# Kernel tuning notes

Measured on AMD Instinct MI355X. Metric: run time of the kernel, lower is better.

## Reference

```python
import jax, jax.numpy as jnp
import numpy as np

B, W, M = 16, 32, 512
NH, HALF, K, H = 64, 32, 8, 8
LK = W // 2               # long-conv kernel size
LOUT = W - 2 * (LK - 1)   # = 2 (dilated valid conv output length)
NSP = 10                  # n_spatial (hardcoded in module)
GC1_IN = (1 + LOUT) * K   # 24


def setup_inputs() -> dict:
    key = jax.random.key(0)
    ks = jax.random.split(key, 23)
    def n(k, shp, s=0.1):
        return jax.random.normal(k, shp, jnp.float32) * s
    return dict(
        x=jax.random.normal(ks[0], (B, W, M), jnp.float32),
        adj=jax.random.uniform(ks[1], (M, M), jnp.float32) / M,  # row-normalized-ish dense adj
        Wih=n(ks[2], (NH, 1)), Whh=n(ks[3], (NH, NH)),
        bih=n(ks[4], (NH,)), bhh=n(ks[5], (NH,)),
        W1=n(ks[6], (HALF, NH)), W2=n(ks[7], (HALF, NH)), b1=n(ks[8], (HALF,)),
        V=n(ks[9], (HALF,)), bv=n(ks[10], (1,)),
        Wb=n(ks[11], (M, M)), wb=n(ks[12], (1,)),
        conv_w=n(ks[13], (K, 1, W)), conv_b=n(ks[14], (K,)),
        convl_w=n(ks[15], (K, 1, LK)), convl_b=n(ks[16], (K,)),
        gc1_w=n(ks[17], (GC1_IN, NH)), gc1_b=n(ks[18], (NH,)),
        gc2_w=n(ks[19], (NH, NSP)), gc2_b=n(ks[20], (NSP,)),
        out_w=n(ks[21], (H, NSP + NH)), out_b=n(ks[22], (H,)),
    )


def reference(x, adj, Wih, Whh, bih, bhh, W1, W2, b1, V, bv, Wb, wb,
              conv_w, conv_b, convl_w, convl_b, gc1_w, gc1_b, gc2_w, gc2_b,
              out_w, out_b):
    b = x.shape[0]
    # [b, w, m] -> per-node sequences [b*m, w]
    seq = jnp.transpose(x, (0, 2, 1)).reshape(b * M, W)

    # vanilla tanh RNN, input_size=1 (batched over all b*m series)
    inp = seq[:, :, None] * Wih[:, 0] + (bih + bhh)          # [b*m, w, nh]
    def step(h, it):
        return jnp.tanh(it + h @ Whh.T), None
    h0 = jnp.zeros((b * M, NH), x.dtype)
    last_hid, _ = jax.lax.scan(step, h0, jnp.swapaxes(inp, 0, 1))
    last_hid = last_hid.reshape(b, M, NH)                    # out_temporal

    # pairwise additive attention: a[b,i,j] = V . elu(W1 h_j + W2 h_i + b1) + bv
    e1 = last_hid @ W1.T                                     # [b, m, half] (j role)
    e2 = last_hid @ W2.T                                     # [b, m, half] (i role)
    a = jax.nn.elu(e2[:, :, None, :] + e1[:, None, :, :] + b1)  # [b,m,m,half]
    a_mx = a @ V + bv                                        # [b, m, m]
    # F.normalize(p=2, dim=1)
    norm = jnp.sqrt(jnp.sum(a_mx * a_mx, axis=1, keepdims=True))
    a_mx = a_mx / jnp.maximum(norm, 1e-12)

    # per-node short conv (kernel == window -> out len 1) as a single matmul
    r_short = seq @ conv_w[:, 0, :].T + conv_b               # [b*m, k]
    # per-node dilated long conv, batched over all b*m series
    r_long = jax.lax.conv_general_dilated(
        seq[:, None, :], convl_w, window_strides=(1,), padding='VALID',
        rhs_dilation=(2,), dimension_numbers=('NCW', 'OIW', 'NCW'))
    r_long = r_long + convl_b[None, :, None]                 # [b*m, k, LOUT]
    r = jnp.concatenate([r_short[:, :, None], r_long], axis=-1)  # [b*m, k, 1+LOUT]
    r = jax.nn.relu(r.reshape(b, M, GC1_IN))

    # gated mix of static normalized adj and learned attention adj
    c = jax.nn.sigmoid(a_mx @ Wb + wb)
    adj_mix = adj[None] * c + a_mx * (1.0 - c)               # [b, m, m]

    # two dense graph conv layers: relu(adj @ (h @ W) + b)
    h1 = jax.nn.relu(adj_mix @ (r @ gc1_w) + gc1_b)          # [b, m, nh]
    out_spatial = jax.nn.relu(adj_mix @ (h1 @ gc2_w) + gc2_b)  # [b, m, nsp]

    feat = jnp.concatenate([out_spatial, last_hid], axis=-1)  # [b, m, nsp+nh]
    out = feat @ out_w.T + out_b                              # [b, m, h]
    return jnp.transpose(out, (0, 2, 1))                      # [b, h, m]
```

## Files before the change

### kernel.cpp

```cpp
#include <hip/hip_runtime.h>


typedef __attribute__((ext_vector_type(8))) short bf16x8;
typedef __attribute__((ext_vector_type(4))) float f32x4;
#define MFMA16 __builtin_amdgcn_mfma_f32_16x16x32_bf16

__device__ __forceinline__ unsigned short f2bf(float f) {
    unsigned u = __float_as_uint(f);
    u += 0x7fff + ((u >> 16) & 1);
    return (unsigned short)(u >> 16);
}
__device__ __forceinline__ float bf2f(unsigned short h) {
    return __uint_as_float(((unsigned)h) << 16);
}
__device__ __forceinline__ float fast_tanh(float x) {
    float e = __expf(2.f * x);
    return 1.f - 2.f / (e + 1.f);
}

__global__ __launch_bounds__(256) void fused1_kernel(
    const float* __restrict__ x, const float* __restrict__ Wih,
    const float* __restrict__ Whh, const float* __restrict__ bih,
    const float* __restrict__ bhh, const float* __restrict__ W1,
    const float* __restrict__ W2, float* __restrict__ lh,
    float* __restrict__ e1, float* __restrict__ e2,
    const float* __restrict__ conv_w, const float* __restrict__ conv_b,
    const float* __restrict__ convl_w, const float* __restrict__ convl_b,
    const float* __restrict__ gc1_w, unsigned short* __restrict__ rgT,
    const float* __restrict__ Wb, unsigned short* __restrict__ WbT,
    float* __restrict__ nrmss)
{
    __shared__ __align__(16) char smem[12160];
    int blk = blockIdx.x, t = threadIdx.x;

    if (blk < 256) {
        int wid = t >> 6, lane = t & 63;
        int rowblk = blk * 32;
        int b = rowblk >> 9, mb = rowblk & 511;
        float* xs = (float*)smem;
        unsigned short* hs = (unsigned short*)(smem + 4096);
        float* rrs = (float*)(smem + 8704);

        for (int u = t; u < 1024; u += 256) {
            int tt = u >> 5, c = u & 31;
            xs[tt * 32 + c] = x[(b * 32 + tt) * 512 + mb + c];
        }
        for (int u = t; u < 2304; u += 256) hs[u] = 0;
        __syncthreads();

        if (wid < 2) {
            int l15 = lane & 15, quad = lane >> 4;
            int row0 = rowblk + wid * 16;
            unsigned short* hw0 = hs + wid * 1152;

            bf16x8 afr[4][2];
#pragma unroll
            for (int mt = 0; mt < 4; ++mt)
#pragma unroll
                for (int hf = 0; hf < 2; ++hf) {
                    const float* src = Whh + (16 * mt + l15) * 64 + 32 * hf + quad * 8;
                    union { bf16x8 v; unsigned short u[8]; } tmp;
#pragma unroll
                    for (int j = 0; j < 8; ++j) tmp.u[j] = f2bf(src[j]);
                    afr[mt][hf] = tmp.v;
                }
            bf16x8 wfr[2][2][2];
#pragma unroll
            for (int e = 0; e < 2; ++e)
#pragma unroll
                for (int nt = 0; nt < 2; ++nt)
#pragma unroll
                    for (int kf = 0; kf < 2; ++kf) {
                        const float* Wsrc = (e ? W2 : W1);
                        const float* src = Wsrc + (16 * nt + l15) * 64 + 32 * kf + quad * 8;
                        union { bf16x8 v; unsigned short u[8]; } tmp;
#pragma unroll
                        for (int j = 0; j < 8; ++j) tmp.u[j] = f2bf(src[j]);
                        wfr[e][nt][kf] = tmp.v;
                    }
            float wihv[4][4], bsv[4][4];
#pragma unroll
            for (int mt = 0; mt < 4; ++mt)
#pragma unroll
                for (int r = 0; r < 4; ++r) {
                    int n = 16 * mt + quad * 4 + r;
                    wihv[mt][r] = Wih[n];
                    bsv[mt][r]  = bih[n] + bhh[n];
                }

            float th[4][4];
            for (int tstep = 0; tstep < 32; ++tstep) {
                bf16x8 b0 = *(bf16x8*)(hw0 + l15 * 72 + quad * 8);
                bf16x8 b1 = *(bf16x8*)(hw0 + l15 * 72 + 32 + quad * 8);
                float xt = xs[tstep * 32 + wid * 16 + l15];
                f32x4 acc[4];
#pragma unroll
                for (int mt = 0; mt < 4; ++mt) {
                    f32x4 z = {0.f, 0.f, 0.f, 0.f};
                    acc[mt] = MFMA16(afr[mt][0], b0, z, 0, 0, 0);
                    acc[mt] = MFMA16(afr[mt][1], b1, acc[mt], 0, 0, 0);
                }
#pragma unroll
                for (int mt = 0; mt < 4; ++mt) {
                    ushort4 hwv;
#pragma unroll
                    for (int r = 0; r < 4; ++r)
                        th[mt][r] = fast_tanh(acc[mt][r] + xt * wihv[mt][r] + bsv[mt][r]);
                    hwv.x = f2bf(th[mt][0]); hwv.y = f2bf(th[mt][1]);
                    hwv.z = f2bf(th[mt][2]); hwv.w = f2bf(th[mt][3]);
                    *(ushort4*)(hw0 + l15 * 72 + 16 * mt + quad * 4) = hwv;
                }
            }
#pragma unroll
            for (int mt = 0; mt < 4; ++mt)
                *(float4*)(lh + (row0 + l15) * 64 + 16 * mt + quad * 4) =
                    make_float4(th[mt][0], th[mt][1], th[mt][2], th[mt][3]);

            bf16x8 a0 = *(bf16x8*)(hw0 + l15 * 72 + quad * 8);
            bf16x8 a1 = *(bf16x8*)(hw0 + l15 * 72 + 32 + quad * 8);
#pragma unroll
            for (int e = 0; e < 2; ++e) {
                float* dst = e ? e2 : e1;
#pragma unroll
                for (int nt = 0; nt < 2; ++nt) {
                    f32x4 z = {0.f, 0.f, 0.f, 0.f};
                    f32x4 ee = MFMA16(a0, wfr[e][nt][0], z, 0, 0, 0);
                    ee = MFMA16(a1, wfr[e][nt][1], ee, 0, 0, 0);
#pragma unroll
                    for (int r = 0; r < 4; ++r)
                        dst[(row0 + quad * 4 + r) * 32 + 16 * nt + l15] = ee[r];
                }
            }
        } else {
            int wid2 = wid - 2;
#pragma unroll
            for (int rep = 0; rep < 2; ++rep) {
                int task = rep * 64 + lane;
                int rl = wid2 * 16 + (task >> 3);
                int k  = task & 7;
                float s = conv_b[k];
                for (int w = 0; w < 32; ++w) s += xs[w * 32 + rl] * conv_w[k * 32 + w];
                float l0 = convl_b[k], l1 = l0;
                for (int tt = 0; tt < 16; ++tt) {
                    float wv = convl_w[k * 16 + tt];
                    l0 += xs[(2 * tt) * 32 + rl] * wv;
                    l1 += xs[(2 * tt + 1) * 32 + rl] * wv;
                }
                rrs[rl * 25 + k * 3 + 0] = fmaxf(s, 0.f);
                rrs[rl * 25 + k * 3 + 1] = fmaxf(l0, 0.f);
                rrs[rl * 25 + k * 3 + 2] = fmaxf(l1, 0.f);
            }
            __builtin_amdgcn_wave_barrier();
            int rl = wid2 * 16 + (lane & 15);
            int nb = lane >> 4;
#pragma unroll
            for (int q = 0; q < 16; ++q) {
                int n = nb * 16 + q;
                float acc = 0.f;
#pragma unroll
                for (int c = 0; c < 24; ++c) acc += rrs[rl * 25 + c] * gc1_w[c * 64 + n];
                rgT[b * 32768 + n * 512 + mb + rl] = f2bf(acc);
            }
        }
    } else if (blk < 512) {
        int bid = blk - 256;
        int nb = (bid & 15) * 32, kb = (bid >> 4) * 32;
        float* tile = (float*)smem;
        for (int u = t; u < 1024; u += 256) {
            int r = u >> 5, c = u & 31;
            tile[r * 33 + c] = Wb[(kb + r) * 512 + nb + c];
        }
        __syncthreads();
        for (int u = t; u < 1024; u += 256) {
            int r = u >> 5, c = u & 31;
            WbT[(nb + r) * 512 + kb + c] = f2bf(tile[c * 33 + r]);
        }
    } else {
        nrmss[(blk - 512) * 256 + t] = 0.f;
    }
}

__global__ __launch_bounds__(256) void amx_kernel(
    const float* __restrict__ e1, const float* __restrict__ e2,
    const float* __restrict__ b1p, const float* __restrict__ Vp,
    const float* __restrict__ bvp, unsigned short* __restrict__ amxb,
    float* __restrict__ nrmss)
{
    int bb = blockIdx.z;
    int i0 = blockIdx.y * 64, j0 = blockIdx.x * 64;
    __shared__ float e2s[64][33], e1s[64][33];
    __shared__ float Vs[32];
    __shared__ float red[16][68];
    int t = threadIdx.x;
    for (int u = t; u < 2048; u += 256) {
        int r = u >> 5, c = u & 31;
        e2s[r][c] = e2[(bb * 512 + i0 + r) * 32 + c];
        e1s[r][c] = e1[(bb * 512 + j0 + r) * 32 + c] + b1p[c];
    }
    if (t < 32) Vs[t] = Vp[t];
    __syncthreads();
    int ti = (t >> 4) * 4, tj = (t & 15) * 4;
    float acc[4][4] = {};
#pragma unroll
    for (int h = 0; h < 32; ++h) {
        float vv = Vs[h];
        float xi[4], yj[4], Exi[4], Eyj[4];
#pragma unroll
        for (int p = 0; p < 4; ++p) { xi[p] = e2s[ti + p][h]; Exi[p] = __expf(xi[p]); }
#pragma unroll
        for (int q = 0; q < 4; ++q) { yj[q] = e1s[tj + q][h]; Eyj[q] = __expf(yj[q]); }
#pragma unroll
        for (int p = 0; p < 4; ++p)
#pragma unroll
            for (int q = 0; q < 4; ++q) {
                float v = xi[p] + yj[q];
                float prod = Exi[p] * Eyj[q];
                float el = v > 0.f ? v : prod - 1.f;
                acc[p][q] += vv * el;
            }
    }
    float bv = bvp[0];
    float ss[4] = {0.f, 0.f, 0.f, 0.f};
#pragma unroll
    for (int p = 0; p < 4; ++p) {
        float v0 = acc[p][0] + bv, v1 = acc[p][1] + bv;
        float v2 = acc[p][2] + bv, v3 = acc[p][3] + bv;
        ushort4 o;
        o.x = f2bf(v0); o.y = f2bf(v1); o.z = f2bf(v2); o.w = f2bf(v3);
        *(ushort4*)(amxb + (bb * 512 + i0 + ti + p) * 512 + j0 + tj) = o;
        ss[0] += v0 * v0; ss[1] += v1 * v1; ss[2] += v2 * v2; ss[3] += v3 * v3;
    }
#pragma unroll
    for (int q = 0; q < 4; ++q) red[t >> 4][tj + q] = ss[q];
    __syncthreads();
    if (t < 64) {
        float s = 0.f;
#pragma unroll
        for (int g = 0; g < 16; ++g) s += red[g][t];
        atomicAdd(&nrmss[bb * 512 + j0 + t], s);
    }
}

__global__ __launch_bounds__(256) void gemm_adjmix_h1(
    const unsigned short* __restrict__ amxb, const unsigned short* __restrict__ WbT,
    const float* __restrict__ wbp, const float* __restrict__ adj,
    const float* __restrict__ nrmss, unsigned short* __restrict__ adjmixb,
    const unsigned short* __restrict__ rgT, const float* __restrict__ gc1_b,
    const float* __restrict__ gc2_w, float* __restrict__ h1g)
{
    const int bb = blockIdx.y;
    const int i0 = blockIdx.x * 32;
    __shared__ __align__(16) char smem[23552];
    short* As = (short*)smem;
    short* Bs = (short*)(smem + 4608);
    float* rn = (float*)(smem + 13824);
    float (*h1s)[72] = (float (*)[72])(smem + 13824);

    const int t = threadIdx.x, w = t >> 6, lane = t & 63;
    const int l15 = lane & 15, quad = lane >> 4;
    const int rh = w & 1, ch = w >> 1;
    const int si = t >> 3, so = t & 7;

    for (int u = t; u < 512; u += 256)
        rn[u] = 1.f / fmaxf(sqrtf(nrmss[bb * 512 + u]), 1e-12f);
    const unsigned short* Ag = amxb + bb * 262144;
    const float wb = wbp[0];

    int4 pa, pb0, pb1;
    {
        pa  = *(const int4*)(Ag + (i0 + si) * 512 + 64 + so * 8);
        pb0 = *(const int4*)(WbT + si * 512 + 64 + so * 8);
        pb1 = *(const int4*)(WbT + (32 + si) * 512 + 64 + so * 8);
    }
    f32x4 acc[2];
    const f32x4 zz = {0.f, 0.f, 0.f, 0.f};
    for (int it = 0; it < 64; ++it) {
        const int j0 = it >> 3, kk = it & 7;
        const int k0 = (j0 * 64 + 64 * (kk + 1)) & 511;
        __syncthreads();
        {
            union { int4 v; unsigned short us[8]; } ur; ur.v = pa;
            union { int4 v; unsigned short us[8]; } ow2;
#pragma unroll
            for (int c = 0; c < 8; ++c)
                ow2.us[c] = f2bf(bf2f(ur.us[c]) * rn[k0 + so * 8 + c]);
            *(int4*)(As + si * 72 + so * 8) = ow2.v;
            *(int4*)(Bs + si * 72 + so * 8) = pb0;
            *(int4*)(Bs + (32 + si) * 72 + so * 8) = pb1;
        }
        if (it < 63) {
            const int itn = it + 1, j0n = itn >> 3, kkn = itn & 7;
            const int k0n = (j0n * 64 + 64 * (kkn + 1)) & 511;
            pa  = *(const int4*)(Ag + (i0 + si) * 512 + k0n + so * 8);
            pb0 = *(const int4*)(WbT + (j0n * 64 + si) * 512 + k0n + so * 8);
            pb1 = *(const int4*)(WbT + (j0n * 64 + 32 + si) * 512 + k0n + so * 8);
        }
        __syncthreads();
        if (kk == 0) { acc[0] = zz; acc[1] = zz; }
        bf16x8 a0 = *(bf16x8*)(As + (16 * rh + l15) * 72 + quad * 8);
        bf16x8 a1 = *(bf16x8*)(As + (16 * rh + l15) * 72 + 32 + quad * 8);
#pragma unroll
        for (int q = 0; q < 2; ++q) {
            int nt = ch * 2 + q;
            bf16x8 b0 = *(bf16x8*)(Bs + (16 * nt + l15) * 72 + quad * 8);
            bf16x8 b1 = *(bf16x8*)(Bs + (16 * nt + l15) * 72 + 32 + quad * 8);
            acc[q] = MFMA16(a0, b0, acc[q], 0, 0, 0);
            acc[q] = MFMA16(a1, b1, acc[q], 0, 0, 0);
        }
        if (kk == 7) {
#pragma unroll
            for (int q = 0; q < 2; ++q)
#pragma unroll
            for (int r = 0; r < 4; ++r) {
                int il = 16 * rh + quad * 4 + r;
                int jl = 16 * (ch * 2 + q) + l15;
                int i = i0 + il, j = j0 * 64 + jl;
                float s  = acc[q][r] + wb;
                float cv = 1.f / (1.f + __expf(-s));
                float am = bf2f((unsigned short)As[il * 72 + jl]);
                float ad = adj[i * 512 + j];
                adjmixb[(bb * 512 + i) * 512 + j] = f2bf(ad * cv + am * (1.f - cv));
            }
        }
    }

    const unsigned short* Ag2 = adjmixb + bb * 262144;
    const unsigned short* Bg2 = rgT + bb * 32768;
    const int rt = w & 1, ntb = (w >> 1) * 2;
    f32x4 acc2[2] = {};
    int4 qa, qb0, qb1;
    {
        qa  = *(const int4*)(Ag2 + (i0 + si) * 512 + so * 8);
        qb0 = *(const int4*)(Bg2 + si * 512 + so * 8);
        qb1 = *(const int4*)(Bg2 + (32 + si) * 512 + so * 8);
    }
    for (int kt = 0; kt < 8; ++kt) {
        __syncthreads();
        *(int4*)(As + si * 72 + so * 8) = qa;
        *(int4*)(Bs + si * 72 + so * 8) = qb0;
        *(int4*)(Bs + (32 + si) * 72 + so * 8) = qb1;
        if (kt < 7) {
            const int k0n = (kt + 1) * 64;
            qa  = *(const int4*)(Ag2 + (i0 + si) * 512 + k0n + so * 8);
            qb0 = *(const int4*)(Bg2 + si * 512 + k0n + so * 8);
            qb1 = *(const int4*)(Bg2 + (32 + si) * 512 + k0n + so * 8);
        }
        __syncthreads();
        bf16x8 a0 = *(bf16x8*)(As + (16 * rt + l15) * 72 + quad * 8);
        bf16x8 a1 = *(bf16x8*)(As + (16 * rt + l15) * 72 + 32 + quad * 8);
#pragma unroll
        for (int q = 0; q < 2; ++q) {
            int nt = ntb + q;
            bf16x8 b0 = *(bf16x8*)(Bs + (16 * nt + l15) * 72 + quad * 8);
            bf16x8 b1 = *(bf16x8*)(Bs + (16 * nt + l15) * 72 + 32 + quad * 8);
            acc2[q] = MFMA16(a0, b0, acc2[q], 0, 0, 0);
            acc2[q] = MFMA16(a1, b1, acc2[q], 0, 0, 0);
        }
    }
#pragma unroll
    for (int q = 0; q < 2; ++q)
#pragma unroll
    for (int r = 0; r < 4; ++r) {
        int il = 16 * rt + quad * 4 + r;
        int j = 16 * (ntb + q) + l15;
        h1s[il][j] = fmaxf(acc2[q][r] + gc1_b[j], 0.f);
    }
    __syncthreads();
    for (int u = t; u < 320; u += 256) {
        int row = u / 10, ns = u - row * 10;
        float a2 = 0.f;
#pragma unroll
        for (int j = 0; j < 64; ++j) a2 += h1s[row][j] * gc2_w[j * 10 + ns];
        h1g[(bb * 512 + i0 + row) * 10 + ns] = a2;
    }
}

__global__ __launch_bounds__(256) void ospout_kernel(
    const unsigned short* __restrict__ adjmix, const float* __restrict__ h1g,
    const float* __restrict__ gc2_b, const float* __restrict__ lh,
    const float* __restrict__ out_w, const float* __restrict__ out_b,
    float* __restrict__ out)
{
    int r0 = blockIdx.x * 16;
    int bb = r0 >> 9;
    int wid = threadIdx.x >> 6, lane = threadIdx.x & 63;
    __shared__ float Bsm[10][512];
    __shared__ float ow[8][80];
    __shared__ float ob[8], g2b[10];
    for (int u = threadIdx.x; u < 5120; u += 256) {
        int k = u / 10, ns = u - k * 10;
        Bsm[ns][k] = h1g[bb * 5120 + u];
    }
    if (threadIdx.x < 8)  ob[threadIdx.x]  = out_b[threadIdx.x];
    if (threadIdx.x < 10) g2b[threadIdx.x] = gc2_b[threadIdx.x];
    for (int u = threadIdx.x; u < 592; u += 256) {
        int hh = u / 74, c = u - hh * 74;
        ow[hh][c] = out_w[u];
    }
    __syncthreads();
#pragma unroll
    for (int half = 0; half < 4; ++half) {
        int row = r0 + half * 4 + wid, m = row & 511;
        const unsigned short* Ar = adjmix + row * 512;
        float a[8];
#pragma unroll
        for (int q = 0; q < 8; ++q) a[q] = bf2f(Ar[lane + 64 * q]);
        float os[10];
#pragma unroll
        for (int ns = 0; ns < 10; ++ns) {
            float s = 0.f;
#pragma unroll
            for (int q = 0; q < 8; ++q) s += a[q] * Bsm[ns][lane + 64 * q];
#pragma unroll
            for (int off = 32; off; off >>= 1) s += __shfl_xor(s, off);
            os[ns] = fmaxf(s + g2b[ns], 0.f);
        }
        float lv = lh[row * 64 + lane];
#pragma unroll
        for (int hh = 0; hh < 8; ++hh) {
            float t1 = lv * ow[hh][10 + lane];
#pragma unroll
            for (int off = 32; off; off >>= 1) t1 += __shfl_xor(t1, off);
            if (lane == hh) {
                float acc = ob[hh] + t1;
#pragma unroll
                for (int ns = 0; ns < 10; ++ns) acc += os[ns] * ow[hh][ns];
                out[bb * 4096 + hh * 512 + m] = acc;
            }
        }
    }
}

extern "C" void kernel_launch(void* const* d_in, const int* in_sizes, int n_in,
                              void* d_out, int out_size, void* d_ws, size_t ws_size,
                              hipStream_t stream)
{
    const float* x       = (const float*)d_in[0];
    const float* adj     = (const float*)d_in[1];
    const float* Wih     = (const float*)d_in[2];
    const float* Whh     = (const float*)d_in[3];
    const float* bih     = (const float*)d_in[4];
    const float* bhh     = (const float*)d_in[5];
    const float* W1      = (const float*)d_in[6];
    const float* W2      = (const float*)d_in[7];
    const float* b1      = (const float*)d_in[8];
    const float* V       = (const float*)d_in[9];
    const float* bv      = (const float*)d_in[10];
    const float* Wb      = (const float*)d_in[11];
    const float* wb      = (const float*)d_in[12];
    const float* conv_w  = (const float*)d_in[13];
    const float* conv_b  = (const float*)d_in[14];
    const float* convl_w = (const float*)d_in[15];
    const float* convl_b = (const float*)d_in[16];
    const float* gc1_w   = (const float*)d_in[17];
    const float* gc1_b   = (const float*)d_in[18];
    const float* gc2_w   = (const float*)d_in[19];
    const float* gc2_b   = (const float*)d_in[20];
    const float* out_w   = (const float*)d_in[21];
    const float* out_b   = (const float*)d_in[22];

    float* ws    = (float*)d_ws;
    float* lh    = ws;
    float* e1    = lh + 524288;
    float* e2    = e1 + 262144;
    float* nrmss = e2 + 262144;
    float* h1g   = nrmss + 8192;
    unsigned short* amxb    = (unsigned short*)(h1g + 81920);
    unsigned short* adjmixb = amxb + 4194304;
    unsigned short* WbT     = adjmixb + 4194304;
    unsigned short* rgT     = WbT + 262144;

    fused1_kernel<<<544, 256, 0, stream>>>(
        x, Wih, Whh, bih, bhh, W1, W2, lh, e1, e2,
        conv_w, conv_b, convl_w, convl_b, gc1_w, rgT, Wb, WbT, nrmss);
    amx_kernel<<<dim3(8, 8, 16), 256, 0, stream>>>(e1, e2, b1, V, bv,
                                                   amxb, nrmss);
    gemm_adjmix_h1<<<dim3(16, 16), 256, 0, stream>>>(
        amxb, WbT, wb, adj, nrmss, adjmixb, rgT, gc1_b, gc2_w, h1g);
    ospout_kernel<<<512, 256, 0, stream>>>(adjmixb, h1g, gc2_b, lh,
                                           out_w, out_b, (float*)d_out);
}
```

Baseline: 220.3 us.

## Restructure adj-mix gate GEMM to register-tiled full-K accumulation without LDS staging

The gate GEMM (a_mx @ Wb) previously recomputed A tiles for each 64-column output chunk, streaming through LDS with barriers per k-step. Now each wave holds a 16x256 output tile in registers (16 accumulators) and loops K once, loading A and WbT fragments directly from global memory. A is normalized and converted to bf16 once per k-step instead of eight times. In exchange it uses many more registers, which may lower occupancy, and relies on cache for WbT reuse across waves.

```diff
diff --git a/kernel.cpp b/kernel.cpp
--- a/kernel.cpp
+++ b/kernel.cpp
@@ -250,83 +250,73 @@
 {
     const int bb = blockIdx.y;
     const int i0 = blockIdx.x * 32;
-    __shared__ __align__(16) char smem[23552];
-    short* As = (short*)smem;
-    short* Bs = (short*)(smem + 4608);
-    float* rn = (float*)(smem + 13824);
-    float (*h1s)[72] = (float (*)[72])(smem + 13824);
+    __shared__ __align__(16) char smem[25088];
+    float* rn = (float*)smem;
+    short* As = (short*)(smem + 2048);
+    short* Bs = (short*)(smem + 6656);
+    float (*h1s)[72] = (float (*)[72])(smem + 15872);
 
     const int t = threadIdx.x, w = t >> 6, lane = t & 63;
     const int l15 = lane & 15, quad = lane >> 4;
-    const int rh = w & 1, ch = w >> 1;
-    const int si = t >> 3, so = t & 7;
 
     for (int u = t; u < 512; u += 256)
         rn[u] = 1.f / fmaxf(sqrtf(nrmss[bb * 512 + u]), 1e-12f);
+    __syncthreads();
+
     const unsigned short* Ag = amxb + bb * 262144;
     const float wb = wbp[0];
-
-    int4 pa, pb0, pb1;
-    {
-        pa  = *(const int4*)(Ag + (i0 + si) * 512 + 64 + so * 8);
-        pb0 = *(const int4*)(WbT + si * 512 + 64 + so * 8);
-        pb1 = *(const int4*)(WbT + (32 + si) * 512 + 64 + so * 8);
-    }
-    f32x4 acc[2];
-    const f32x4 zz = {0.f, 0.f, 0.f, 0.f};
-    for (int it = 0; it < 64; ++it) {
-        const int j0 = it >> 3, kk = it & 7;
-        const int k0 = (j0 * 64 + 64 * (kk + 1)) & 511;
-        __syncthreads();
+    const int rowb = i0 + 16 * (w & 1);
+    const int colb = 256 * (w >> 1);
+
+    f32x4 acc[4][4] = {};
+    const unsigned short* Arow = Ag + (rowb + l15) * 512;
+    for (int k0 = 0; k0 < 512; k0 += 64) {
+        bf16x8 a0, a1;
         {
-            union { int4 v; unsigned short us[8]; } ur; ur.v = pa;
-            union { int4 v; unsigned short us[8]; } ow2;
-#pragma unroll
-            for (int c = 0; c < 8; ++c)
-                ow2.us[c] = f2bf(bf2f(ur.us[c]) * rn[k0 + so * 8 + c]);
-            *(int4*)(As + si * 72 + so * 8) = ow2.v;
-            *(int4*)(Bs + si * 72 + so * 8) = pb0;
-            *(int4*)(Bs + (32 + si) * 72 + so * 8) = pb1;
-        }
-        if (it < 63) {
-            const int itn = it + 1, j0n = itn >> 3, kkn = itn & 7;
-            const int k0n = (j0n * 64 + 64 * (kkn + 1)) & 511;
-            pa  = *(const int4*)(Ag + (i0 + si) * 512 + k0n + so * 8);
-            pb0 = *(const int4*)(WbT + (j0n * 64 + si) * 512 + k0n + so * 8);
-            pb1 = *(const int4*)(WbT + (j0n * 64 + 32 + si) * 512 + k0n + so * 8);
-        }
-        __syncthreads();
-        if (kk == 0) { acc[0] = zz; acc[1] = zz; }
-        bf16x8 a0 = *(bf16x8*)(As + (16 * rh + l15) * 72 + quad * 8);
-        bf16x8 a1 = *(bf16x8*)(As + (16 * rh + l15) * 72 + 32 + quad * 8);
-#pragma unroll
-        for (int q = 0; q < 2; ++q) {
-            int nt = ch * 2 + q;
-            bf16x8 b0 = *(bf16x8*)(Bs + (16 * nt + l15) * 72 + quad * 8);
-            bf16x8 b1 = *(bf16x8*)(Bs + (16 * nt + l15) * 72 + 32 + quad * 8);
-            acc[q] = MFMA16(a0, b0, acc[q], 0, 0, 0);
-            acc[q] = MFMA16(a1, b1, acc[q], 0, 0, 0);
-        }
-        if (kk == 7) {
-#pragma unroll
-            for (int q = 0; q < 2; ++q)
-#pragma unroll
-            for (int r = 0; r < 4; ++r) {
-                int il = 16 * rh + quad * 4 + r;
-                int jl = 16 * (ch * 2 + q) + l15;
-                int i = i0 + il, j = j0 * 64 + jl;
-                float s  = acc[q][r] + wb;
-                float cv = 1.f / (1.f + __expf(-s));
-                float am = bf2f((unsigned short)As[il * 72 + jl]);
-                float ad = adj[i * 512 + j];
-                adjmixb[(bb * 512 + i) * 512 + j] = f2bf(ad * cv + am * (1.f - cv));
-            }
-        }
-    }
+            union { int4 v; unsigned short us[8]; } r0, r1;
+            r0.v = *(const int4*)(Arow + k0 + quad * 8);
+            r1.v = *(const int4*)(Arow + k0 + 32 + quad * 8);
+            union { bf16x8 v; unsigned short us[8]; } o0, o1;
+            const float* rn0 = rn + k0 + quad * 8;
+#pragma unroll
+            for (int c = 0; c < 8; ++c) {
+                o0.us[c] = f2bf(bf2f(r0.us[c]) * rn0[c]);
+                o1.us[c] = f2bf(bf2f(r1.us[c]) * rn0[32 + c]);
+            }
+            a0 = o0.v; a1 = o1.v;
+        }
+#pragma unroll
+        for (int j64 = 0; j64 < 4; ++j64)
+#pragma unroll
+        for (int nt = 0; nt < 4; ++nt) {
+            const unsigned short* Brow =
+                WbT + (colb + j64 * 64 + nt * 16 + l15) * 512 + k0;
+            bf16x8 b0 = *(const bf16x8*)(Brow + quad * 8);
+            bf16x8 b1 = *(const bf16x8*)(Brow + 32 + quad * 8);
+            acc[j64][nt] = MFMA16(a0, b0, acc[j64][nt], 0, 0, 0);
+            acc[j64][nt] = MFMA16(a1, b1, acc[j64][nt], 0, 0, 0);
+        }
+    }
+#pragma unroll
+    for (int j64 = 0; j64 < 4; ++j64)
+#pragma unroll
+    for (int nt = 0; nt < 4; ++nt)
+#pragma unroll
+    for (int r = 0; r < 4; ++r) {
+        int i = rowb + quad * 4 + r;
+        int j = colb + j64 * 64 + nt * 16 + l15;
+        float s  = acc[j64][nt][r] + wb;
+        float cv = 1.f / (1.f + __expf(-s));
+        float am = bf2f(f2bf(bf2f(Ag[i * 512 + j]) * rn[j]));
+        float ad = adj[i * 512 + j];
+        adjmixb[(bb * 512 + i) * 512 + j] = f2bf(ad * cv + am * (1.f - cv));
+    }
+    __syncthreads();
 
     const unsigned short* Ag2 = adjmixb + bb * 262144;
     const unsigned short* Bg2 = rgT + bb * 32768;
     const int rt = w & 1, ntb = (w >> 1) * 2;
+    const int si = t >> 3, so = t & 7;
     f32x4 acc2[2] = {};
     int4 qa, qb0, qb1;
     {
```

Result: slower. 245.0 us (+11.2%).
